# Kernel optimization log

Hardware: AMD Instinct MI355X
Metric: run time of the kernel (lower is better)

## Reference

```python
import jax, jax.numpy as jnp
import numpy as np

B, T, C, H, W = 1, 16, 320, 16, 16
HEADS, DIM_HEAD, NREG = 8, 40, 1
L = T * H * W  # 4096


def setup_inputs() -> dict:
    key = jax.random.key(0)
    ks = jax.random.split(key, 8)
    features = jax.random.normal(ks[0], (B, T, C, H, W), jnp.float32)
    # epipolar geometry mask: True = attend. randint 0/1 per spec.
    attn_mask = jax.random.randint(ks[1], (B, L, L), 0, 2) == 1
    s = 0.02
    Wq = jax.random.normal(ks[2], (C, HEADS * DIM_HEAD), jnp.float32) * s
    Wk = jax.random.normal(ks[3], (C, HEADS * DIM_HEAD), jnp.float32) * s
    Wv = jax.random.normal(ks[4], (C, HEADS * DIM_HEAD), jnp.float32) * s
    reg_tokens = jax.random.normal(ks[5], (1, NREG, C), jnp.float32)
    Wo = jax.random.normal(ks[6], (HEADS * DIM_HEAD, C), jnp.float32) * s
    bo = jnp.zeros((C,), jnp.float32)
    return {"features": features, "attn_mask": attn_mask, "Wq": Wq, "Wk": Wk,
            "Wv": Wv, "reg_tokens": reg_tokens, "Wo": Wo, "bo": bo}


def reference(features, attn_mask, Wq, Wk, Wv, reg_tokens, Wo, bo):
    b, t, c, h, w = features.shape
    # B T C H W -> B (T H W) C
    x = features.transpose(0, 1, 3, 4, 2).reshape(b, t * h * w, c)
    context = jnp.concatenate(
        [jnp.broadcast_to(reg_tokens, (b, NREG, c)), x], axis=1)
    # pad mask: register tokens always visible (True)
    mask = jnp.pad(attn_mask, ((0, 0), (0, 0), (NREG, 0)), constant_values=True)
    # projections, split heads: B L (H D) -> B H L D
    def heads(y):
        return y.reshape(b, y.shape[1], HEADS, DIM_HEAD).transpose(0, 2, 1, 3)
    q = heads(x @ Wq)
    k = heads(context @ Wk)
    v = heads(context @ Wv)
    scale = DIM_HEAD ** -0.5  # SDPA default scale
    scores = jnp.einsum('bhqd,bhkd->bhqk', q, k) * scale
    neg = jnp.finfo(scores.dtype).min
    scores = jnp.where(mask[:, None, :, :], scores, neg)
    attn = jax.nn.softmax(scores, axis=-1)
    out = jnp.einsum('bhqk,bhkd->bhqd', attn, v)
    out = out.transpose(0, 2, 1, 3).reshape(b, t * h * w, HEADS * DIM_HEAD)
    out = out @ Wo + bo
    # B (T H W) C -> (B H W) T C
    out = out.reshape(b, t, h, w, c).transpose(0, 2, 3, 1, 4)
    return out.reshape(b * h * w, t, c)
```

## Files before the change

### kernel.cpp

```cpp
#include <hip/hip_runtime.h>
#include <hip/hip_bf16.h>
#include <math.h>

#define CDIM 320
#define LQ   4096
#define LKTX 4097
#define NH   8
#define DH   40
#define NWORDS 65
#define NSPLIT 4
#define CBROWS 4224

typedef __attribute__((ext_vector_type(8))) short short8;
typedef __attribute__((ext_vector_type(4))) short short4v;
typedef __attribute__((ext_vector_type(4))) float f32x4;

#define MFMA16(a, b, c) __builtin_amdgcn_mfma_f32_16x16x16bf16_1k(a, b, c, 0, 0, 0)
#define MFMA32(a, b, c) __builtin_amdgcn_mfma_f32_16x16x32_bf16(a, b, c, 0, 0, 0)

#define QSCALE ((float)(0.15811388300841897 * 1.4426950408889634))

__global__ __launch_bounds__(256) void prep(
    const float* __restrict__ feat, const float* __restrict__ reg,
    const float* __restrict__ Wq, const float* __restrict__ Wk,
    const float* __restrict__ Wv, const float* __restrict__ Wo,
    const int* __restrict__ mask, unsigned long long* __restrict__ packed,
    __hip_bfloat16* __restrict__ ctxb, __hip_bfloat16* __restrict__ Wt,
    __hip_bfloat16* __restrict__ Wot) {
    __shared__ float xs[64 * 65];
    int b = blockIdx.x, t = threadIdx.x;
    if (b < 16384) {
        int wid = b * 4 + (t >> 6);
        int j = t & 63;
        int q = wid >> 4, g = wid & 15;
        const uint4* m4 = (const uint4*)(mask + (size_t)q * 4096 + g * 256);
        uint4 mv = m4[j];
        unsigned long long b0 = __ballot(mv.x != 0);
        unsigned long long b1 = __ballot(mv.y != 0);
        unsigned long long b2 = __ballot(mv.z != 0);
        unsigned long long b3 = __ballot(mv.w != 0);
        unsigned long long carry =
            (g == 0) ? 1ull
                     : (unsigned long long)(mask[(size_t)q * 4096 + g * 256 - 1] != 0);
        unsigned long long b3s = (b3 << 1) | carry;
        if (j < 4) {
            int sh = j * 16;
            unsigned long long w = ((b3s >> sh) & 0xFFFFull) |
                                   (((b0 >> sh) & 0xFFFFull) << 16) |
                                   (((b1 >> sh) & 0xFFFFull) << 32) |
                                   (((b2 >> sh) & 0xFFFFull) << 48);
            packed[(size_t)q * NWORDS + g * 4 + j] = w;
        }
        if (j == 4 && g == 15) packed[(size_t)q * NWORDS + 64] = b3 >> 63;
    } else if (b < 16704) {
        int bb = b - 16384;
        int tt = bb & 15, cg = (bb >> 4) % 5, hg = (bb >> 4) / 5;
        int c0 = cg * 64, hw0 = hg * 64;
        int cl = t >> 6, hwl = t & 63;
#pragma unroll
        for (int i = 0; i < 16; i++) {
            int c = cl * 16 + i;
            xs[c * 65 + hwl] = feat[(size_t)(tt * CDIM + c0 + c) * 256 + hw0 + hwl];
        }
        __syncthreads();
        int cq = t >> 6;
        int row = tt * 256 + hw0 + hwl;
        short8 v0, v1;
#pragma unroll
        for (int j = 0; j < 8; j++) {
            __hip_bfloat16 b0 = __float2bfloat16(xs[(cq * 16 + j) * 65 + hwl]);
            __hip_bfloat16 b1 = __float2bfloat16(xs[(cq * 16 + 8 + j) * 65 + hwl]);
            v0[j] = *(short*)&b0;
            v1[j] = *(short*)&b1;
        }
        short* dst = (short*)ctxb + (size_t)(1 + row) * CDIM + c0 + cq * 16;
        *(short8*)dst = v0;
        *(short8*)(dst + 8) = v1;
    } else {
        int idx = (b - 16704) * 256 + t;
        if (idx < 960 * 320) {
            int n = idx / 320, k = idx % 320;
            float v;
            if (n < 320)      v = Wq[k * 320 + n] * QSCALE;
            else if (n < 640) v = Wk[k * 320 + (n - 320)];
            else              v = Wv[k * 320 + (n - 640)];
            Wt[n * 320 + k] = __float2bfloat16(v);
        }
        if (idx < 320 * 320) {
            int n = idx / 320, k = idx % 320;
            Wot[n * 320 + k] = __float2bfloat16(Wo[k * 320 + n]);
        }
        if (idx < 320) ctxb[idx] = __float2bfloat16(reg[idx]);
    }
}

__global__ __launch_bounds__(256) void qkv_gemm(
    const __hip_bfloat16* __restrict__ Ab, const __hip_bfloat16* __restrict__ Btb,
    __hip_bfloat16* __restrict__ Cbo) {
    __shared__ short As[64 * 72];
    __shared__ short Bs[128 * 72];
    const short* A  = (const short*)Ab;
    const short* Bt = (const short*)Btb;
    int t = threadIdx.x;
    int wv = t >> 6, lane = t & 63, quad = lane >> 4, l16 = lane & 15;
    int m0 = blockIdx.y * 64, n0 = blockIdx.x * 128;

    f32x4 acc[8];
#pragma unroll
    for (int ct = 0; ct < 8; ct++)
#pragma unroll
        for (int r = 0; r < 4; r++) acc[ct][r] = 0.f;

    for (int k0 = 0; k0 < 320; k0 += 64) {
        uint4 av[2], bv[4];
#pragma unroll
        for (int i = 0; i < 2; i++) {
            int c = t + i * 256;
            int row = c >> 3, kc = (c & 7) * 8;
            av[i] = make_uint4(0, 0, 0, 0);
            if (m0 + row < LKTX)
                av[i] = *(const uint4*)(A + (size_t)(m0 + row) * 320 + k0 + kc);
        }
#pragma unroll
        for (int i = 0; i < 4; i++) {
            int c = t + i * 256;
            int row = c >> 3, kc = (c & 7) * 8;
            bv[i] = make_uint4(0, 0, 0, 0);
            if (n0 + row < 960)
                bv[i] = *(const uint4*)(Bt + (size_t)(n0 + row) * 320 + k0 + kc);
        }
        __syncthreads();
#pragma unroll
        for (int i = 0; i < 2; i++) {
            int c = t + i * 256;
            *(uint4*)&As[(c >> 3) * 72 + (c & 7) * 8] = av[i];
        }
#pragma unroll
        for (int i = 0; i < 4; i++) {
            int c = t + i * 256;
            *(uint4*)&Bs[(c >> 3) * 72 + (c & 7) * 8] = bv[i];
        }
        __syncthreads();
        short8 a0 = *(const short8*)&As[(wv * 16 + l16) * 72 + quad * 8];
        short8 a1 = *(const short8*)&As[(wv * 16 + l16) * 72 + 32 + quad * 8];
#pragma unroll
        for (int ct = 0; ct < 8; ct++) {
            short8 b0 = *(const short8*)&Bs[(ct * 16 + l16) * 72 + quad * 8];
            short8 b1 = *(const short8*)&Bs[(ct * 16 + l16) * 72 + 32 + quad * 8];
            acc[ct] = MFMA32(a0, b0, acc[ct]);
            acc[ct] = MFMA32(a1, b1, acc[ct]);
        }
        __syncthreads();
    }
#pragma unroll
    for (int ct = 0; ct < 8; ct++)
#pragma unroll
        for (int r = 0; r < 4; r++) {
            int m = m0 + wv * 16 + quad * 4 + r;
            int n = n0 + ct * 16 + l16;
            if (n < 960)
                Cbo[(size_t)m * 960 + n] = __float2bfloat16(acc[ct][r]);
        }
}

__global__ __launch_bounds__(256, 4) void flash_attn(
    const __hip_bfloat16* __restrict__ Cbh,
    const unsigned long long* __restrict__ packed,
    float* __restrict__ Opart, float* __restrict__ l_arr) {
    __shared__ short Ks[2 * 64 * 72];
    __shared__ short Vs[2 * 48 * 72];

    int t = threadIdx.x;
    int wv = t >> 6, lane = t & 63;
    int quad = lane >> 4, l16 = lane & 15;
    int h = blockIdx.y, s = blockIdx.z;
    int q0 = blockIdx.x * 128 + wv * 32;
    int kt0 = (s == 0) ? 0 : 16 * s + 1;
    int nkt = s ? 16 : 17;
    const short* Cb = (const short*)Cbh;

    for (int i = t; i < 64 * 24; i += 256) {
        int rr = i / 24, c = 40 + i % 24;
        Ks[rr * 72 + c] = 0;
        Ks[4608 + rr * 72 + c] = 0;
    }
    for (int i = t; i < 8 * 72; i += 256) {
        int rr = i / 72, c = i % 72;
        short v = (rr == 0 && c < 64) ? (short)0x3F80 : (short)0;
        Vs[(40 + rr) * 72 + c] = v;
        Vs[3456 + (40 + rr) * 72 + c] = v;
    }

    short8 qa[2][2];
#pragma unroll
    for (int qs = 0; qs < 2; qs++) {
        const short* qp = Cb + (size_t)(q0 + qs * 16 + l16 + 1) * 960 + h * DH;
        qa[qs][0] = *(const short8*)(qp + quad * 8);
        short8 z = {0, 0, 0, 0, 0, 0, 0, 0};
        qa[qs][1] = (quad == 0) ? *(const short8*)(qp + 32) : z;
    }

    int key0 = t / 5, cc0 = t - 5 * key0;
    int t2 = t + 256;
    int key1 = t2 / 5, cc1 = t2 - 5 * key1;
    bool has2 = (t < 64);
    const short* pK0 = Cb + (size_t)(kt0 * 64 + key0) * 960 + 320 + h * DH + cc0 * 8;
    const short* pV0 = Cb + (size_t)(kt0 * 64 + key0) * 960 + 640 + h * DH + cc0 * 8;
    const short* pK1 = Cb + (size_t)(kt0 * 64 + key1) * 960 + 320 + h * DH + cc1 * 8;
    const short* pV1 = Cb + (size_t)(kt0 * 64 + key1) * 960 + 640 + h * DH + cc1 * 8;
    const unsigned long long* pM0 = packed + (size_t)(q0 + l16) * NWORDS + kt0;
    const unsigned long long* pM1 = packed + (size_t)(q0 + 16 + l16) * NWORDS + kt0;

    uint4 rk0 = *(const uint4*)pK0;  pK0 += 61440;
    uint4 rv0 = *(const uint4*)pV0;  pV0 += 61440;
    uint4 rk1 = make_uint4(0, 0, 0, 0), rv1 = make_uint4(0, 0, 0, 0);
    if (has2) { rk1 = *(const uint4*)pK1; rv1 = *(const uint4*)pV1; }
    pK1 += 61440; pV1 += 61440;
    unsigned long long wq0 = *pM0++;
    unsigned long long wq1 = *pM1++;

    f32x4 accO[2][3];
#pragma unroll
    for (int qs = 0; qs < 2; qs++)
#pragma unroll
        for (int dt = 0; dt < 3; dt++)
#pragma unroll
            for (int r = 0; r < 4; r++) accO[qs][dt][r] = 0.f;

    for (int it = 0; it < nkt; it++) {
        int ko = (it & 1) * 4608, vo = (it & 1) * 3456;
        *(uint4*)&Ks[ko + key0 * 72 + cc0 * 8] = rk0;
        {
            const short* ds = (const short*)&rv0;
#pragma unroll
            for (int u = 0; u < 8; u++) Vs[vo + (cc0 * 8 + u) * 72 + key0] = ds[u];
        }
        if (has2) {
            *(uint4*)&Ks[ko + key1 * 72 + cc1 * 8] = rk1;
            const short* ds = (const short*)&rv1;
#pragma unroll
            for (int u = 0; u < 8; u++) Vs[vo + (cc1 * 8 + u) * 72 + key1] = ds[u];
        }
        unsigned long long mw0 = wq0, mw1 = wq1;
        rk0 = *(const uint4*)pK0;  pK0 += 61440;
        rv0 = *(const uint4*)pV0;  pV0 += 61440;
        if (has2) { rk1 = *(const uint4*)pK1; rv1 = *(const uint4*)pV1; }
        pK1 += 61440; pV1 += 61440;
        wq0 = *pM0++;
        wq1 = *pM1++;
        __syncthreads();

        const short* KB = &Ks[ko];
        const short* VB = &Vs[vo];
        unsigned lo[2], hi[2];
        lo[0] = (unsigned)(mw0 >> quad);
        hi[0] = (unsigned)(mw0 >> (quad + 32));
        lo[1] = (unsigned)(mw1 >> quad);
        hi[1] = (unsigned)(mw1 >> (quad + 32));

        short4v pf[2][4];
#pragma unroll
        for (int ct = 0; ct < 4; ct++) {
            short8 kb0 = *(const short8*)&KB[(ct * 16 + l16) * 72 + quad * 8];
            short8 kb1 = *(const short8*)&KB[(ct * 16 + l16) * 72 + 32 + quad * 8];
#pragma unroll
            for (int qs = 0; qs < 2; qs++) {
                f32x4 S = {0.f, 0.f, 0.f, 0.f};
                S = MFMA32(kb0, qa[qs][0], S);
                S = MFMA32(kb1, qa[qs][1], S);
                float p0 = __builtin_amdgcn_exp2f(S[0]);
                float p1 = __builtin_amdgcn_exp2f(S[1]);
                float p2 = __builtin_amdgcn_exp2f(S[2]);
                float p3 = __builtin_amdgcn_exp2f(S[3]);
                p0 = ((lo[qs] >> (4 * ct)) & 1u) ? p0 : 0.f;
                p1 = ((lo[qs] >> (4 * ct + 16)) & 1u) ? p1 : 0.f;
                p2 = ((hi[qs] >> (4 * ct)) & 1u) ? p2 : 0.f;
                p3 = ((hi[qs] >> (4 * ct + 16)) & 1u) ? p3 : 0.f;
                unsigned u0 = __float_as_uint(p0) + 0x8000u;
                unsigned u1 = __float_as_uint(p1) + 0x8000u;
                unsigned u2 = __float_as_uint(p2) + 0x8000u;
                unsigned u3 = __float_as_uint(p3) + 0x8000u;
                uint2 pk = make_uint2((u0 >> 16) | (u1 & 0xFFFF0000u),
                                      (u2 >> 16) | (u3 & 0xFFFF0000u));
                pf[qs][ct] = *(short4v*)&pk;
            }
        }

#pragma unroll
        for (int dt = 0; dt < 3; dt++) {
#pragma unroll
            for (int ct = 0; ct < 4; ct++) {
                short4v vf = *(const short4v*)&VB[(dt * 16 + l16) * 72 + ct * 16 + quad * 4];
                accO[0][dt] = MFMA16(vf, pf[0][ct], accO[0][dt]);
                accO[1][dt] = MFMA16(vf, pf[1][ct], accO[1][dt]);
            }
        }
    }

#pragma unroll
    for (int qs = 0; qs < 2; qs++) {
        int q = q0 + qs * 16 + l16;
        size_t base = ((size_t)(s * NH + h) * LQ + q) * DH;
        float4 f0 = make_float4(accO[qs][0][0], accO[qs][0][1], accO[qs][0][2], accO[qs][0][3]);
        float4 f1 = make_float4(accO[qs][1][0], accO[qs][1][1], accO[qs][1][2], accO[qs][1][3]);
        *(float4*)&Opart[base + quad * 4] = f0;
        *(float4*)&Opart[base + 16 + quad * 4] = f1;
        if (quad < 2) {
            float4 f2 = make_float4(accO[qs][2][0], accO[qs][2][1], accO[qs][2][2], accO[qs][2][3]);
            *(float4*)&Opart[base + 32 + quad * 4] = f2;
        }
        if (quad == 2) l_arr[(size_t)(s * NH + h) * LQ + q] = accO[qs][2][0];
    }
}

__global__ __launch_bounds__(256) void out_gemm(
    const float* __restrict__ Opart, const float* __restrict__ l_arr,
    const __hip_bfloat16* __restrict__ Wotb, float* __restrict__ C,
    const float* __restrict__ bias) {
    __shared__ short As[64 * 72];
    __shared__ short Bs[64 * 72];
    const short* Bt = (const short*)Wotb;
    int t = threadIdx.x;
    int wv = t >> 6, lane = t & 63, quad = lane >> 4, l16 = lane & 15;
    int m0 = blockIdx.y * 64, n0 = blockIdx.x * 64;

    f32x4 acc[4];
#pragma unroll
    for (int ct = 0; ct < 4; ct++)
#pragma unroll
        for (int r = 0; r < 4; r++) acc[ct][r] = 0.f;

    for (int k0 = 0; k0 < 5; k0++) {
        uint4 av[2], bv[2];
#pragma unroll
        for (int i = 0; i < 2; i++) {
            int cidx = t + i * 256;
            int row = cidx >> 3, cl = (cidx & 7) * 8;
            int c = k0 * 64 + cl;
            int hh = c / 40, d = c % 40;
            int q = m0 + row;
            float ls = 0.f;
            float vals[8] = {0, 0, 0, 0, 0, 0, 0, 0};
#pragma unroll
            for (int sp = 0; sp < NSPLIT; sp++) {
                size_t rbase = ((size_t)(sp * NH + hh) * LQ + q) * DH + d;
                float4 a = *(const float4*)&Opart[rbase];
                float4 b = *(const float4*)&Opart[rbase + 4];
                vals[0] += a.x; vals[1] += a.y; vals[2] += a.z; vals[3] += a.w;
                vals[4] += b.x; vals[5] += b.y; vals[6] += b.z; vals[7] += b.w;
                ls += l_arr[(size_t)(sp * NH + hh) * LQ + q];
            }
            float inv = 1.f / ls;
            unsigned pk[4];
#pragma unroll
            for (int u = 0; u < 4; u++) {
                unsigned e0 = __float_as_uint(vals[2 * u] * inv) + 0x8000u;
                unsigned e1 = __float_as_uint(vals[2 * u + 1] * inv) + 0x8000u;
                pk[u] = (e0 >> 16) | (e1 & 0xFFFF0000u);
            }
            av[i] = make_uint4(pk[0], pk[1], pk[2], pk[3]);
            bv[i] = *(const uint4*)(Bt + (size_t)(n0 + row) * 320 + k0 * 64 + cl);
        }
        __syncthreads();
#pragma unroll
        for (int i = 0; i < 2; i++) {
            int cidx = t + i * 256;
            *(uint4*)&As[(cidx >> 3) * 72 + (cidx & 7) * 8] = av[i];
            *(uint4*)&Bs[(cidx >> 3) * 72 + (cidx & 7) * 8] = bv[i];
        }
        __syncthreads();
        short8 a0 = *(const short8*)&As[(wv * 16 + l16) * 72 + quad * 8];
        short8 a1 = *(const short8*)&As[(wv * 16 + l16) * 72 + 32 + quad * 8];
#pragma unroll
        for (int ct = 0; ct < 4; ct++) {
            short8 b0 = *(const short8*)&Bs[(ct * 16 + l16) * 72 + quad * 8];
            short8 b1 = *(const short8*)&Bs[(ct * 16 + l16) * 72 + 32 + quad * 8];
            acc[ct] = MFMA32(a0, b0, acc[ct]);
            acc[ct] = MFMA32(a1, b1, acc[ct]);
        }
        __syncthreads();
    }
#pragma unroll
    for (int ct = 0; ct < 4; ct++)
#pragma unroll
        for (int r = 0; r < 4; r++) {
            int m = m0 + wv * 16 + quad * 4 + r;
            int n = n0 + ct * 16 + l16;
            int rp = (m & 255) * 16 + (m >> 8);
            C[(size_t)rp * CDIM + n] = acc[ct][r] + bias[n];
        }
}

extern "C" void kernel_launch(void* const* d_in, const int* in_sizes, int n_in,
                              void* d_out, int out_size, void* d_ws, size_t ws_size,
                              hipStream_t stream) {
    const float* feat = (const float*)d_in[0];
    const int*   mask = (const int*)d_in[1];
    const float* Wq   = (const float*)d_in[2];
    const float* Wk   = (const float*)d_in[3];
    const float* Wv   = (const float*)d_in[4];
    const float* reg  = (const float*)d_in[5];
    const float* Wo   = (const float*)d_in[6];
    const float* bo   = (const float*)d_in[7];
    float* out = (float*)d_out;

    char* p = (char*)d_ws;
    auto alloc = [&](size_t bytes) {
        char* r = p;
        p += (bytes + 255) & ~(size_t)255;
        return r;
    };
    __hip_bfloat16* ctxb = (__hip_bfloat16*)alloc((size_t)LKTX * CDIM * 2);
    __hip_bfloat16* Cb   = (__hip_bfloat16*)alloc((size_t)CBROWS * 960 * 2);
    __hip_bfloat16* Wt   = (__hip_bfloat16*)alloc((size_t)960 * 320 * 2);
    __hip_bfloat16* Wot  = (__hip_bfloat16*)alloc((size_t)320 * 320 * 2);
    unsigned long long* packed =
        (unsigned long long*)alloc(((size_t)LQ * NWORDS + 64) * 8);
    float* Opart = (float*)alloc((size_t)NSPLIT * NH * LQ * DH * 4);
    float* l_arr = (float*)alloc((size_t)NSPLIT * NH * LQ * 4);

    prep<<<17904, 256, 0, stream>>>(feat, reg, Wq, Wk, Wv, Wo, mask, packed,
                                    ctxb, Wt, Wot);
    qkv_gemm<<<dim3(8, 65), 256, 0, stream>>>(ctxb, Wt, Cb);
    flash_attn<<<dim3(32, NH, NSPLIT), 256, 0, stream>>>(Cb, packed, Opart, l_arr);
    out_gemm<<<dim3(5, 64), 256, 0, stream>>>(Opart, l_arr, Wot, out, bo);
}
```

Before: 221.3 us.

## Widen out_gemm N tile, pad V LDS stride to 68, interleave PV MFMAs

In out_gemm each block now covers 160 output columns instead of 64, so the expensive split-reduction and normalisation of Opart into bf16 A tiles is done 2 times per row block instead of 5. In flash_attn the V shared-memory row stride drops from 72 to 68 shorts to change the bank pattern of the transposed V stores. The QK MFMAs for both query sub-tiles are issued back-to-back, and the PV MFMAs for each key chunk run right after its probabilities are formed, which shortens the live range of the P fragments. Risks: more accumulator registers and fewer blocks in out_gemm, and possible misaligned or conflicting 8-byte V reads at the new stride.

```diff
diff --git a/kernel.cpp b/kernel.cpp
--- a/kernel.cpp
+++ b/kernel.cpp
@@ -168,7 +168,7 @@
     const unsigned long long* __restrict__ packed,
     float* __restrict__ Opart, float* __restrict__ l_arr) {
     __shared__ short Ks[2 * 64 * 72];
-    __shared__ short Vs[2 * 48 * 72];
+    __shared__ short Vs[2 * 48 * 68];
 
     int t = threadIdx.x;
     int wv = t >> 6, lane = t & 63;
@@ -182,13 +182,13 @@
     for (int i = t; i < 64 * 24; i += 256) {
         int rr = i / 24, c = 40 + i % 24;
         Ks[rr * 72 + c] = 0;
-        Ks[4608 + rr * 72 + c] = 0;
-    }
-    for (int i = t; i < 8 * 72; i += 256) {
-        int rr = i / 72, c = i % 72;
+        Ks[64 * 72 + rr * 72 + c] = 0;
+    }
+    for (int i = t; i < 8 * 68; i += 256) {
+        int rr = i / 68, c = i % 68;
         short v = (rr == 0 && c < 64) ? (short)0x3F80 : (short)0;
-        Vs[(40 + rr) * 72 + c] = v;
-        Vs[3456 + (40 + rr) * 72 + c] = v;
+        Vs[(40 + rr) * 68 + c] = v;
+        Vs[48 * 68 + (40 + rr) * 68 + c] = v;
     }
 
     short8 qa[2][2];
@@ -228,18 +228,18 @@
             for (int r = 0; r < 4; r++) accO[qs][dt][r] = 0.f;
 
     for (int it = 0; it < nkt; it++) {
-        int ko = (it & 1) * 4608, vo = (it & 1) * 3456;
+        int ko = (it & 1) * (64 * 72), vo = (it & 1) * (48 * 68);
         *(uint4*)&Ks[ko + key0 * 72 + cc0 * 8] = rk0;
         {
             const short* ds = (const short*)&rv0;
 #pragma unroll
-            for (int u = 0; u < 8; u++) Vs[vo + (cc0 * 8 + u) * 72 + key0] = ds[u];
+            for (int u = 0; u < 8; u++) Vs[vo + (cc0 * 8 + u) * 68 + key0] = ds[u];
         }
         if (has2) {
             *(uint4*)&Ks[ko + key1 * 72 + cc1 * 8] = rk1;
             const short* ds = (const short*)&rv1;
 #pragma unroll
-            for (int u = 0; u < 8; u++) Vs[vo + (cc1 * 8 + u) * 72 + key1] = ds[u];
+            for (int u = 0; u < 8; u++) Vs[vo + (cc1 * 8 + u) * 68 + key1] = ds[u];
         }
         unsigned long long mw0 = wq0, mw1 = wq1;
         rk0 = *(const uint4*)pK0;  pK0 += 61440;
@@ -258,20 +258,24 @@
         lo[1] = (unsigned)(mw1 >> quad);
         hi[1] = (unsigned)(mw1 >> (quad + 32));
 
-        short4v pf[2][4];
 #pragma unroll
         for (int ct = 0; ct < 4; ct++) {
             short8 kb0 = *(const short8*)&KB[(ct * 16 + l16) * 72 + quad * 8];
             short8 kb1 = *(const short8*)&KB[(ct * 16 + l16) * 72 + 32 + quad * 8];
+            f32x4 S[2];
+            S[0] = f32x4{0.f, 0.f, 0.f, 0.f};
+            S[1] = f32x4{0.f, 0.f, 0.f, 0.f};
+            S[0] = MFMA32(kb0, qa[0][0], S[0]);
+            S[0] = MFMA32(kb1, qa[0][1], S[0]);
+            S[1] = MFMA32(kb0, qa[1][0], S[1]);
+            S[1] = MFMA32(kb1, qa[1][1], S[1]);
+            short4v pf[2];
 #pragma unroll
             for (int qs = 0; qs < 2; qs++) {
-                f32x4 S = {0.f, 0.f, 0.f, 0.f};
-                S = MFMA32(kb0, qa[qs][0], S);
-                S = MFMA32(kb1, qa[qs][1], S);
-                float p0 = __builtin_amdgcn_exp2f(S[0]);
-                float p1 = __builtin_amdgcn_exp2f(S[1]);
-                float p2 = __builtin_amdgcn_exp2f(S[2]);
-                float p3 = __builtin_amdgcn_exp2f(S[3]);
+                float p0 = __builtin_amdgcn_exp2f(S[qs][0]);
+                float p1 = __builtin_amdgcn_exp2f(S[qs][1]);
+                float p2 = __builtin_amdgcn_exp2f(S[qs][2]);
+                float p3 = __builtin_amdgcn_exp2f(S[qs][3]);
                 p0 = ((lo[qs] >> (4 * ct)) & 1u) ? p0 : 0.f;
                 p1 = ((lo[qs] >> (4 * ct + 16)) & 1u) ? p1 : 0.f;
                 p2 = ((hi[qs] >> (4 * ct)) & 1u) ? p2 : 0.f;
@@ -282,17 +286,13 @@
                 unsigned u3 = __float_as_uint(p3) + 0x8000u;
                 uint2 pk = make_uint2((u0 >> 16) | (u1 & 0xFFFF0000u),
                                       (u2 >> 16) | (u3 & 0xFFFF0000u));
-                pf[qs][ct] = *(short4v*)&pk;
+                pf[qs] = *(short4v*)&pk;
             }
-        }
-
-#pragma unroll
-        for (int dt = 0; dt < 3; dt++) {
-#pragma unroll
-            for (int ct = 0; ct < 4; ct++) {
-                short4v vf = *(const short4v*)&VB[(dt * 16 + l16) * 72 + ct * 16 + quad * 4];
-                accO[0][dt] = MFMA16(vf, pf[0][ct], accO[0][dt]);
-                accO[1][dt] = MFMA16(vf, pf[1][ct], accO[1][dt]);
+#pragma unroll
+            for (int dt = 0; dt < 3; dt++) {
+                short4v vf = *(const short4v*)&VB[(dt * 16 + l16) * 68 + ct * 16 + quad * 4];
+                accO[0][dt] = MFMA16(vf, pf[0], accO[0][dt]);
+                accO[1][dt] = MFMA16(vf, pf[1], accO[1][dt]);
             }
         }
     }
@@ -318,20 +318,20 @@
     const __hip_bfloat16* __restrict__ Wotb, float* __restrict__ C,
     const float* __restrict__ bias) {
     __shared__ short As[64 * 72];
-    __shared__ short Bs[64 * 72];
+    __shared__ short Bs[160 * 72];
     const short* Bt = (const short*)Wotb;
     int t = threadIdx.x;
     int wv = t >> 6, lane = t & 63, quad = lane >> 4, l16 = lane & 15;
-    int m0 = blockIdx.y * 64, n0 = blockIdx.x * 64;
-
-    f32x4 acc[4];
-#pragma unroll
-    for (int ct = 0; ct < 4; ct++)
+    int m0 = blockIdx.y * 64, n0 = blockIdx.x * 160;
+
+    f32x4 acc[10];
+#pragma unroll
+    for (int ct = 0; ct < 10; ct++)
 #pragma unroll
         for (int r = 0; r < 4; r++) acc[ct][r] = 0.f;
 
     for (int k0 = 0; k0 < 5; k0++) {
-        uint4 av[2], bv[2];
+        uint4 av[2], bv[5];
 #pragma unroll
         for (int i = 0; i < 2; i++) {
             int cidx = t + i * 256;
@@ -345,9 +345,9 @@
             for (int sp = 0; sp < NSPLIT; sp++) {
                 size_t rbase = ((size_t)(sp * NH + hh) * LQ + q) * DH + d;
                 float4 a = *(const float4*)&Opart[rbase];
-                float4 b = *(const float4*)&Opart[rbase + 4];
+                float4 b2 = *(const float4*)&Opart[rbase + 4];
                 vals[0] += a.x; vals[1] += a.y; vals[2] += a.z; vals[3] += a.w;
-                vals[4] += b.x; vals[5] += b.y; vals[6] += b.z; vals[7] += b.w;
+                vals[4] += b2.x; vals[5] += b2.y; vals[6] += b2.z; vals[7] += b2.w;
                 ls += l_arr[(size_t)(sp * NH + hh) * LQ + q];
             }
             float inv = 1.f / ls;
@@ -359,20 +359,29 @@
                 pk[u] = (e0 >> 16) | (e1 & 0xFFFF0000u);
             }
             av[i] = make_uint4(pk[0], pk[1], pk[2], pk[3]);
-            bv[i] = *(const uint4*)(Bt + (size_t)(n0 + row) * 320 + k0 * 64 + cl);
+        }
+#pragma unroll
+        for (int i = 0; i < 5; i++) {
+            int cidx = t + i * 256;
+            int row = cidx >> 3, kc = (cidx & 7) * 8;
+            bv[i] = *(const uint4*)(Bt + (size_t)(n0 + row) * 320 + k0 * 64 + kc);
         }
         __syncthreads();
 #pragma unroll
         for (int i = 0; i < 2; i++) {
             int cidx = t + i * 256;
             *(uint4*)&As[(cidx >> 3) * 72 + (cidx & 7) * 8] = av[i];
+        }
+#pragma unroll
+        for (int i = 0; i < 5; i++) {
+            int cidx = t + i * 256;
             *(uint4*)&Bs[(cidx >> 3) * 72 + (cidx & 7) * 8] = bv[i];
         }
         __syncthreads();
         short8 a0 = *(const short8*)&As[(wv * 16 + l16) * 72 + quad * 8];
         short8 a1 = *(const short8*)&As[(wv * 16 + l16) * 72 + 32 + quad * 8];
 #pragma unroll
-        for (int ct = 0; ct < 4; ct++) {
+        for (int ct = 0; ct < 10; ct++) {
             short8 b0 = *(const short8*)&Bs[(ct * 16 + l16) * 72 + quad * 8];
             short8 b1 = *(const short8*)&Bs[(ct * 16 + l16) * 72 + 32 + quad * 8];
             acc[ct] = MFMA32(a0, b0, acc[ct]);
@@ -381,7 +390,7 @@
         __syncthreads();
     }
 #pragma unroll
-    for (int ct = 0; ct < 4; ct++)
+    for (int ct = 0; ct < 10; ct++)
 #pragma unroll
         for (int r = 0; r < 4; r++) {
             int m = m0 + wv * 16 + quad * 4 + r;
@@ -423,5 +432,5 @@
                                     ctxb, Wt, Wot);
     qkv_gemm<<<dim3(8, 65), 256, 0, stream>>>(ctxb, Wt, Cb);
     flash_attn<<<dim3(32, NH, NSPLIT), 256, 0, stream>>>(Cb, packed, Opart, l_arr);
-    out_gemm<<<dim3(5, 64), 256, 0, stream>>>(Opart, l_arr, Wot, out, bo);
+    out_gemm<<<dim3(2, 64), 256, 0, stream>>>(Opart, l_arr, Wot, out, bo);
 }
```

After: 211.7 us. 1.05x faster.
